# Kernel optimization log

Measured on AMD Instinct MI355X. Metric: run time of the kernel, lower is better.

## Reference

```python
import jax, jax.numpy as jnp
import numpy as np
from jax import lax

T_STEPS = 10       # fixed unroll length in forward (range(10))
TASK = 16          # params['task_size']
FEAT = 256         # input_size - task_size
VOCAB = 128        # params['vocab_size']
SH = 512           # sender_hidden_size
RH = 512           # receiver_hidden_size
ND = 10            # num_digits
B = 16384          # batch_size


def _gru_step(h, x, Wih, Whh, bih, bhh):
    # PyTorch GRU/GRUCell equations. Wih: [3H, In], Whh: [3H, H]
    gi = x @ Wih.T + bih
    gh = h @ Whh.T + bhh
    ir, iz, inn = jnp.split(gi, 3, axis=-1)
    hr, hz, hn = jnp.split(gh, 3, axis=-1)
    r = jax.nn.sigmoid(ir + hr)
    z = jax.nn.sigmoid(iz + hz)
    n = jnp.tanh(inn + r * hn)
    return (1.0 - z) * n + z * h


def setup_inputs() -> dict:
    key = jax.random.key(0)
    ks = jax.random.split(key, 16)
    s = 0.05
    x = jax.random.normal(ks[0], (B, TASK + FEAT), jnp.float32)
    u = jax.random.uniform(ks[1], (T_STEPS, B, VOCAB), jnp.float32, 1e-6, 1.0 - 1e-6)
    gumbel = -jnp.log(-jnp.log(u))  # standard Gumbel noise, fixed for determinism
    inp = {
        "x": x,
        "gumbel": gumbel,
        "W_in": jax.random.normal(ks[2], (SH, FEAT), jnp.float32) * s,
        "b_in": jnp.zeros((SH,), jnp.float32),
        "Wih_s": jax.random.normal(ks[3], (3 * SH, VOCAB), jnp.float32) * s,
        "Whh_s": jax.random.normal(ks[4], (3 * SH, SH), jnp.float32) * s,
        "bih_s": jnp.zeros((3 * SH,), jnp.float32),
        "bhh_s": jnp.zeros((3 * SH,), jnp.float32),
        "W_sp": jax.random.normal(ks[5], (VOCAB, SH), jnp.float32) * s,
        "b_sp": jnp.zeros((VOCAB,), jnp.float32),
        "Wih_r": jax.random.normal(ks[6], (3 * RH, VOCAB), jnp.float32) * s,
        "Whh_r": jax.random.normal(ks[7], (3 * RH, RH), jnp.float32) * s,
        "bih_r": jnp.zeros((3 * RH,), jnp.float32),
        "bhh_r": jnp.zeros((3 * RH,), jnp.float32),
        "W_c": jax.random.normal(ks[8], (ND, RH + TASK), jnp.float32) * s,
        "b_c": jnp.zeros((ND,), jnp.float32),
    }
    return inp


def _forward(x, gumbel, W_in, b_in, Wih_s, Whh_s, bih_s, bhh_s, W_sp, b_sp,
             Wih_r, Whh_r, bih_r, bhh_r, W_c, b_c):
    feats = x[:, TASK:]
    task = x[:, :TASK]
    h0 = jnp.tanh(feats @ W_in.T + b_in)                      # [B, SH]
    inp0 = jnp.zeros((x.shape[0], VOCAB), x.dtype)

    def sender_step(carry, g):
        h, w = carry
        h = _gru_step(h, w, Wih_s, Whh_s, bih_s, bhh_s)
        logits = h @ W_sp.T + b_sp
        y_soft = jax.nn.softmax(logits + g, axis=-1)          # gumbel_softmax, tau=1
        onehot = jax.nn.one_hot(jnp.argmax(y_soft, axis=-1), VOCAB, dtype=y_soft.dtype)
        y = onehot + y_soft - lax.stop_gradient(y_soft)       # hard straight-through
        return (h, lax.stop_gradient(y)), y                   # input_word = y.detach()

    (_, _), output_words = lax.scan(sender_step, (h0, inp0), gumbel)  # [10, B, V]

    # cumulative stop-token masking: once argmax==0 at step i-1, zero all steps >= i
    words = jnp.argmax(output_words, axis=2)                  # [10, B]
    nz = (words != 0).astype(output_words.dtype)
    alive = jnp.concatenate(
        [jnp.ones((1, words.shape[1]), output_words.dtype), jnp.cumprod(nz[:-1], axis=0)],
        axis=0)                                               # [10, B]
    masked = output_words * alive[:, :, None]

    # receiver GRU, zero initial hidden, return final hidden
    hr0 = jnp.zeros((x.shape[0], RH), x.dtype)

    def recv_step(h, w):
        h = _gru_step(h, w, Wih_r, Whh_r, bih_r, bhh_r)
        return h, None

    h_n, _ = lax.scan(recv_step, hr0, masked)                 # [B, RH]
    score = jnp.concatenate([h_n, task], axis=1) @ W_c.T + b_c  # [B, ND]
    return score


def reference(x, gumbel, W_in, b_in, Wih_s, Whh_s, bih_s, bhh_s, W_sp, b_sp,
              Wih_r, Whh_r, bih_r, bhh_r, W_c, b_c):
    return _forward(x, gumbel, W_in, b_in, Wih_s, Whh_s, bih_s, bhh_s, W_sp, b_sp,
                    Wih_r, Whh_r, bih_r, bhh_r, W_c, b_c)
```

## Files before the change

kernel.cpp:

```cpp
#include <hip/hip_runtime.h>
#include <math.h>

#define NB 16384
#define NT 10

typedef _Float16 f16;
typedef f16 f16x8 __attribute__((ext_vector_type(8)));
typedef f16 f16x4 __attribute__((ext_vector_type(4)));
typedef float f32x4 __attribute__((ext_vector_type(4)));

__device__ __forceinline__ float sigm_mid(float v) { return 1.0f / (1.0f + __expf(-v)); }
__device__ __forceinline__ float tanh_mid(float v) { return 1.0f - 2.0f / (1.0f + __expf(2.0f * v)); }
__device__ __forceinline__ float sigm_fast(float v) {
    return __builtin_amdgcn_rcpf(1.0f + __expf(-v));
}
__device__ __forceinline__ float tanh_fast(float v) {
    return 1.0f - 2.0f * __builtin_amdgcn_rcpf(1.0f + __expf(2.0f * v));
}

__device__ __forceinline__ void async_cp16(const f16* g, f16* l) {
    __builtin_amdgcn_global_load_lds(
        (const __attribute__((address_space(1))) unsigned int*)g,
        (__attribute__((address_space(3))) unsigned int*)l, 16, 0, 0);
}

__global__ __launch_bounds__(256) void wsplit_kernel(
    const float* __restrict__ W, f16* __restrict__ whi, f16* __restrict__ wlo,
    int rows, int kstride)
{
    const int u = blockIdx.x * 256 + threadIdx.x;
    const int kg = u / rows, row = u - kg * rows;
    const float* s = W + (size_t)row * kstride + kg * 8;
    f16x8 hi8, lo8;
    #pragma unroll
    for (int i = 0; i < 8; ++i) {
        float v = s[i];
        f16 hv = (f16)v;
        hi8[i] = hv;
        lo8[i] = (f16)(v - (float)hv);
    }
    *(f16x8*)&whi[(size_t)u * 8] = hi8;
    *(f16x8*)&wlo[(size_t)u * 8] = lo8;
}

__global__ __launch_bounds__(256) void xsplit_kernel(
    const float* __restrict__ x, f16* __restrict__ xhi, f16* __restrict__ xlo)
{
    const int u = blockIdx.x * 256 + threadIdx.x;
    const int kg = u >> 14, row = u & (NB - 1);
    const float* s = x + (size_t)row * 272 + 16 + kg * 8;
    f16x8 hi8, lo8;
    #pragma unroll
    for (int i = 0; i < 8; ++i) {
        float v = s[i];
        f16 hv = (f16)v;
        hi8[i] = hv;
        lo8[i] = (f16)(v - (float)hv);
    }
    *(f16x8*)&xhi[(size_t)u * 8] = hi8;
    *(f16x8*)&xlo[(size_t)u * 8] = lo8;
}

__global__ __launch_bounds__(256) void wihT_kernel(
    const float* __restrict__ Wih, float* __restrict__ WihT)
{
    const int u = blockIdx.x * 256 + threadIdx.x;
    const int w = u / 1536, c = u - w * 1536;
    WihT[u] = Wih[(size_t)c * 128 + w];
}

__global__ __launch_bounds__(256, 2) void h0_mfma(
    const f16* __restrict__ xs_hi, const f16* __restrict__ xs_lo,
    const f16* __restrict__ win_hi, const f16* __restrict__ win_lo,
    const float* __restrict__ bias, f16* __restrict__ h_hi, f16* __restrict__ h_lo)
{
    constexpr int UNITS = 1536;
    __shared__ __align__(16) f16 lds[2 * UNITS * 8];
    const int t = threadIdx.x;
    const int lane = t & 63, wave = t >> 6;
    const int wm = wave >> 1, wn = wave & 1;
    const int nid = (blockIdx.x & 7) * 128 + (blockIdx.x >> 3);
    const int m0 = (nid >> 3) * 128;
    const int n0 = (nid & 7) * 64;
    const int wbase = t & 192;

    const f32x4 z4 = {0.f, 0.f, 0.f, 0.f};
    f32x4 acc[4][2];
    #pragma unroll
    for (int mi = 0; mi < 4; ++mi)
        #pragma unroll
        for (int ni = 0; ni < 2; ++ni) acc[mi][ni] = z4;

    const int asel = ((lane >> 4) << 7) + wm * 64 + (lane & 15);
    const int bsel = ((lane >> 4) << 6) + wn * 32 + (lane & 15);

    const f16* sp[6];
    #pragma unroll
    for (int i = 0; i < 6; ++i) {
        const int u = i * 256 + t;
        const f16* src;
        if (u < 512) {
            src = xs_hi + ((size_t)(u >> 7) * NB + m0 + (u & 127)) * 8;
        } else if (u < 1024) {
            const int v = u - 512;
            src = xs_lo + ((size_t)(v >> 7) * NB + m0 + (v & 127)) * 8;
        } else if (u < 1280) {
            const int v = u - 1024;
            src = win_hi + ((size_t)(v >> 6) * 512 + n0 + (v & 63)) * 8;
        } else {
            const int v = u - 1280;
            src = win_lo + ((size_t)(v >> 6) * 512 + n0 + (v & 63)) * 8;
        }
        sp[i] = src;
    }

    #define H0_STAGE(buf_) { \
        f16* lb_ = lds + ((size_t)(buf_) * UNITS + wbase) * 8; \
        _Pragma("unroll") \
        for (int i = 0; i < 6; ++i) { \
            async_cp16(sp[i], lb_ + (size_t)i * 256 * 8); \
            sp[i] += (i < 4) ? (size_t)NB * 32 : (size_t)16384; \
        } \
    }

    H0_STAGE(0);
    asm volatile("s_waitcnt vmcnt(0)" ::: "memory");
    __syncthreads();

    for (int kb = 0; kb < 8; ++kb) {
        if (kb < 7) H0_STAGE((kb + 1) & 1);

        const f16* lb = lds + (size_t)(kb & 1) * UNITS * 8;
        f16x8 ah[4], al[4];
        #pragma unroll
        for (int mi = 0; mi < 4; ++mi) {
            ah[mi] = *(const f16x8*)&lb[(size_t)(asel + mi * 16) * 8];
            al[mi] = *(const f16x8*)&lb[(size_t)(512 + asel + mi * 16) * 8];
        }
        f16x8 bh[2], bl[2];
        #pragma unroll
        for (int ni = 0; ni < 2; ++ni) {
            bh[ni] = *(const f16x8*)&lb[(size_t)(1024 + bsel + ni * 16) * 8];
            bl[ni] = *(const f16x8*)&lb[(size_t)(1280 + bsel + ni * 16) * 8];
        }
        #pragma unroll
        for (int mi = 0; mi < 4; ++mi)
            #pragma unroll
            for (int ni = 0; ni < 2; ++ni) {
                acc[mi][ni] = __builtin_amdgcn_mfma_f32_16x16x32_f16(ah[mi], bh[ni], acc[mi][ni], 0, 0, 0);
                acc[mi][ni] = __builtin_amdgcn_mfma_f32_16x16x32_f16(ah[mi], bl[ni], acc[mi][ni], 0, 0, 0);
                acc[mi][ni] = __builtin_amdgcn_mfma_f32_16x16x32_f16(al[mi], bh[ni], acc[mi][ni], 0, 0, 0);
            }
        __syncthreads();
    }

    const int colb = n0 + wn * 32 + (lane & 15);
    const int rowb = m0 + wm * 64 + ((lane >> 4) << 2);
    #pragma unroll
    for (int ni = 0; ni < 2; ++ni) {
        const int col = colb + ni * 16;
        const float bb = bias[col];
        const size_t cbase = (size_t)(col >> 3) * NB * 8 + (col & 7);
        #pragma unroll
        for (int mi = 0; mi < 4; ++mi) {
            #pragma unroll
            for (int j = 0; j < 4; ++j) {
                const int r = rowb + mi * 16 + j;
                const float o = tanhf(acc[mi][ni][j] + bb);
                const f16 hh = (f16)o;
                const size_t idx = cbase + (size_t)r * 8;
                h_hi[idx] = hh;
                h_lo[idx] = (f16)(o - (float)hh);
            }
        }
    }
}

#define INIT_SP() { \
    _Pragma("unroll") \
    for (int i = 0; i < NST; ++i) { \
        const int u = i * 256 + t; \
        const f16* src; \
        if (PURE) { \
            if (u < 512) { \
                src = hc_hi + ((size_t)(u >> 7) * NB + m0 + (u & 127)) * 8; \
            } else { \
                const int w = u - 512; \
                src = w_hi + ((size_t)((w >> 6) & 3) * 1536 + (w >> 8) * 512 + n0 + (w & 63)) * 8; \
            } \
        } else { \
            if (u < 1024) { \
                const int v = u & 511; \
                const f16* hp = (u < 512) ? hc_hi : hc_lo; \
                src = hp + ((size_t)(v >> 7) * NB + m0 + (v & 127)) * 8; \
            } else { \
                const int v = u - 1024; \
                const f16* wp = (v < 768) ? w_hi : w_lo; \
                const int w = (v < 768) ? v : v - 768; \
                src = wp + ((size_t)((w >> 6) & 3) * 1536 + (w >> 8) * 512 + n0 + (w & 63)) * 8; \
            } \
        } \
        sp[i] = src; \
    } \
}
#define STAGE(buf_) { \
    f16* lb_ = lds + ((size_t)(buf_) * UNITS + wbase) * 8; \
    _Pragma("unroll") \
    for (int i = 0; i < NST; ++i) { \
        async_cp16(sp[i], lb_ + (size_t)i * 256 * 8); \
        sp[i] += (i < HCNT) ? (size_t)NB * 32 : (size_t)49152; \
    } \
}

template <int HZERO, int PURE>
__global__ __launch_bounds__(256, 2) void fused_gru(
    const f16* __restrict__ hc_hi, const f16* __restrict__ hc_lo,
    f16* __restrict__ hn_hi, f16* __restrict__ hn_lo,
    const f16* __restrict__ w_hi, const f16* __restrict__ w_lo,
    const float* __restrict__ WihT,
    const float* __restrict__ bih, const float* __restrict__ bhh,
    const int* __restrict__ wsel)
{
    constexpr int UNITS = PURE ? 1280 : 2560;
    constexpr int NST = PURE ? 5 : 10;
    constexpr int HCNT = PURE ? 2 : 4;
    __shared__ __align__(16) f16 lds[2 * UNITS * 8];
    const int t = threadIdx.x;
    const int lane = t & 63, wave = t >> 6;
    const int wm = wave >> 1, wn = wave & 1;
    const int nid = (blockIdx.x & 7) * 128 + (blockIdx.x >> 3);
    const int m0 = (nid >> 3) * 128;
    const int n0 = (nid & 7) * 64;
    const int wbase = t & 192;

    const f32x4 z4 = {0.f, 0.f, 0.f, 0.f};
    f32x4 acc[3][4][2];
    #pragma unroll
    for (int g = 0; g < 3; ++g)
        #pragma unroll
        for (int mi = 0; mi < 4; ++mi)
            #pragma unroll
            for (int ni = 0; ni < 2; ++ni) acc[g][mi][ni] = z4;

    float hold[2][4][4];
    #pragma unroll
    for (int ni = 0; ni < 2; ++ni)
        #pragma unroll
        for (int mi = 0; mi < 4; ++mi)
            #pragma unroll
            for (int j = 0; j < 4; ++j) hold[ni][mi][j] = 0.f;

    if (!HZERO) {
        const int asel = ((lane >> 4) << 7) + wm * 64 + (lane & 15);
        const int bsel = ((lane >> 4) << 6) + wn * 32 + (lane & 15);
        constexpr int B0 = PURE ? 512 : 1024;
        const int kbE = (n0 >> 5) + wn;
        const int kglA = (lane & 15) >> 3;
        const int rowlA = wm * 64 + ((lane >> 4) << 2);
        const int elemA = lane & 7;

        const f16* sp[NST];
        INIT_SP();
        STAGE(0);
        asm volatile("s_waitcnt vmcnt(0)" ::: "memory");
        __syncthreads();

        for (int kb = 0; kb < 16; ++kb) {
            if (kb < 15) STAGE((kb + 1) & 1);

            const f16* lb = lds + (size_t)(kb & 1) * UNITS * 8;
            f16x8 ah[4], al[4];
            #pragma unroll
            for (int mi = 0; mi < 4; ++mi) {
                ah[mi] = *(const f16x8*)&lb[(size_t)(asel + mi * 16) * 8];
                if (!PURE) al[mi] = *(const f16x8*)&lb[(size_t)(512 + asel + mi * 16) * 8];
            }
            #pragma unroll
            for (int g = 0; g < 3; ++g) {
                f16x8 bh[2], bl[2];
                #pragma unroll
                for (int ni = 0; ni < 2; ++ni) {
                    bh[ni] = *(const f16x8*)&lb[(size_t)(B0 + g * 256 + bsel + ni * 16) * 8];
                    if (!PURE) bl[ni] = *(const f16x8*)&lb[(size_t)(1792 + g * 256 + bsel + ni * 16) * 8];
                }
                #pragma unroll
                for (int mi = 0; mi < 4; ++mi)
                    #pragma unroll
                    for (int ni = 0; ni < 2; ++ni) {
                        acc[g][mi][ni] = __builtin_amdgcn_mfma_f32_16x16x32_f16(ah[mi], bh[ni], acc[g][mi][ni], 0, 0, 0);
                        if (!PURE) {
                            acc[g][mi][ni] = __builtin_amdgcn_mfma_f32_16x16x32_f16(ah[mi], bl[ni], acc[g][mi][ni], 0, 0, 0);
                            acc[g][mi][ni] = __builtin_amdgcn_mfma_f32_16x16x32_f16(al[mi], bh[ni], acc[g][mi][ni], 0, 0, 0);
                        }
                    }
            }

            if (kb == kbE) {
                #pragma unroll
                for (int ni = 0; ni < 2; ++ni)
                    #pragma unroll
                    for (int mi = 0; mi < 4; ++mi)
                        #pragma unroll
                        for (int j = 0; j < 4; ++j) {
                            const int unit = (kglA + 2 * ni) * 128 + rowlA + mi * 16 + j;
                            float hv = (float)lb[(size_t)unit * 8 + elemA];
                            if (!PURE) hv += (float)lb[(size_t)(512 + unit) * 8 + elemA];
                            hold[ni][mi][j] = hv;
                        }
            }
            __syncthreads();
        }
    }

    const int colb = n0 + wn * 32 + (lane & 15);
    const int rowb = m0 + wm * 64 + ((lane >> 4) << 2);
    int wd[16];
    if (wsel) {
        #pragma unroll
        for (int mi = 0; mi < 4; ++mi) {
            const int4 w4 = *(const int4*)&wsel[rowb + mi * 16];
            wd[mi * 4 + 0] = w4.x; wd[mi * 4 + 1] = w4.y;
            wd[mi * 4 + 2] = w4.z; wd[mi * 4 + 3] = w4.w;
        }
    } else {
        #pragma unroll
        for (int i = 0; i < 16; ++i) wd[i] = -1;
    }

    #pragma unroll
    for (int ni = 0; ni < 2; ++ni) {
        const int col = colb + ni * 16;
        const float b_r = bih[col], b_z = bih[512 + col], b_n = bih[1024 + col];
        const float c_r = bhh[col], c_z = bhh[512 + col], c_n = bhh[1024 + col];
        const size_t cbase = (size_t)(col >> 3) * NB * 8 + (col & 7);
        #pragma unroll
        for (int mi = 0; mi < 4; ++mi) {
            #pragma unroll
            for (int j = 0; j < 4; ++j) {
                const int r = rowb + mi * 16 + j;
                const int word = wd[mi * 4 + j];
                float wir = 0.f, wiz = 0.f, win = 0.f;
                if (word >= 0) {
                    const float* wt = WihT + (size_t)word * 1536 + col;
                    wir = wt[0]; wiz = wt[512]; win = wt[1024];
                }
                const size_t idx = cbase + (size_t)r * 8;
                const float ra = wir + b_r + acc[0][mi][ni][j] + c_r;
                const float za = wiz + b_z + acc[1][mi][ni][j] + c_z;
                const float rr = PURE ? sigm_fast(ra) : sigm_mid(ra);
                const float zz = PURE ? sigm_fast(za) : sigm_mid(za);
                const float na = win + b_n + rr * (acc[2][mi][ni][j] + c_n);
                const float nn = PURE ? tanh_fast(na) : tanh_mid(na);
                const float hv = (1.f - zz) * nn + zz * hold[ni][mi][j];
                const f16 hh = (f16)hv;
                hn_hi[idx] = hh;
                if (!PURE) hn_lo[idx] = (f16)(hv - (float)hh);
            }
        }
    }
}

__global__ __launch_bounds__(256, 2) void argmax_mfma(
    const f16* __restrict__ h_hi, const f16* __restrict__ h_lo,
    const f16* __restrict__ wsp_hi, const f16* __restrict__ wsp_lo,
    const float* __restrict__ bsp, const float* __restrict__ gum,
    int* __restrict__ wout)
{
    __shared__ __align__(16) f16 lds[2 * 1536 * 8];
    const int t = threadIdx.x;
    const int lane = t & 63, wave = t >> 6;
    const int mBase = blockIdx.x * 64;

    const f32x4 z4 = {0.f, 0.f, 0.f, 0.f};
    f32x4 acc[8];
    #pragma unroll
    for (int nf = 0; nf < 8; ++nf) acc[nf] = z4;

    const f16* sp[6];
    sp[0] = h_hi   + ((size_t)(t >> 6) * NB + mBase + (t & 63)) * 8;
    sp[1] = h_lo   + ((size_t)(t >> 6) * NB + mBase + (t & 63)) * 8;
    sp[2] = wsp_hi + ((size_t)(t >> 7) * 128 + (t & 127)) * 8;
    sp[3] = wsp_hi + ((size_t)(2 + (t >> 7)) * 128 + (t & 127)) * 8;
    sp[4] = wsp_lo + ((size_t)(t >> 7) * 128 + (t & 127)) * 8;
    sp[5] = wsp_lo + ((size_t)(2 + (t >> 7)) * 128 + (t & 127)) * 8;

    f16x8 st[6];
    #pragma unroll
    for (int i = 0; i < 6; ++i) {
        st[i] = *(const f16x8*)sp[i];
        sp[i] += (i < 2) ? (size_t)NB * 32 : (size_t)4096;
    }

    const int aselU = (lane >> 4) * 64 + wave * 16 + (lane & 15);
    const int bselU = 512 + (lane >> 4) * 128 + (lane & 15);

    for (int kb = 0; kb < 16; ++kb) {
        f16* lb = lds + (size_t)(kb & 1) * 1536 * 8;
        #pragma unroll
        for (int i = 0; i < 6; ++i)
            *(f16x8*)&lb[(size_t)(i * 256 + t) * 8] = st[i];
        __syncthreads();
        if (kb < 15) {
            #pragma unroll
            for (int i = 0; i < 6; ++i) {
                st[i] = *(const f16x8*)sp[i];
                sp[i] += (i < 2) ? (size_t)NB * 32 : (size_t)4096;
            }
        }

        f16x8 ah = *(const f16x8*)&lb[(size_t)aselU * 8];
        f16x8 al = *(const f16x8*)&lb[(size_t)(256 + aselU) * 8];
        #pragma unroll
        for (int nf = 0; nf < 8; ++nf) {
            f16x8 bh = *(const f16x8*)&lb[(size_t)(bselU + nf * 16) * 8];
            f16x8 bl = *(const f16x8*)&lb[(size_t)(512 + bselU + nf * 16) * 8];
            acc[nf] = __builtin_amdgcn_mfma_f32_16x16x32_f16(ah, bh, acc[nf], 0, 0, 0);
            acc[nf] = __builtin_amdgcn_mfma_f32_16x16x32_f16(ah, bl, acc[nf], 0, 0, 0);
            acc[nf] = __builtin_amdgcn_mfma_f32_16x16x32_f16(al, bh, acc[nf], 0, 0, 0);
        }
    }

    float bv[4];
    int bi[4];
    #pragma unroll
    for (int j = 0; j < 4; ++j) { bv[j] = -1e30f; bi[j] = 0; }
    const int rw0 = mBase + wave * 16 + ((lane >> 4) << 2);
    #pragma unroll
    for (int nf = 0; nf < 8; ++nf) {
        const int col = (lane & 15) + nf * 16;
        const float bb = bsp[col];
        #pragma unroll
        for (int j = 0; j < 4; ++j) {
            const float v = acc[nf][j] + bb + gum[(size_t)(rw0 + j) * 128 + col];
            if (v > bv[j] || (v == bv[j] && col < bi[j])) { bv[j] = v; bi[j] = col; }
        }
    }
    #pragma unroll
    for (int j = 0; j < 4; ++j) {
        #pragma unroll
        for (int off = 1; off <= 8; off <<= 1) {
            const float ov = __shfl_xor(bv[j], off, 64);
            const int oi = __shfl_xor(bi[j], off, 64);
            if (ov > bv[j] || (ov == bv[j] && oi < bi[j])) { bv[j] = ov; bi[j] = oi; }
        }
        if ((lane & 15) == 0) wout[rw0 + j] = bi[j];
    }
}

__global__ __launch_bounds__(256) void eff_kernel(
    const int* __restrict__ words, int* __restrict__ eff)
{
    const int b = blockIdx.x * 256 + threadIdx.x;
    int alive = 1;
    #pragma unroll
    for (int t = 0; t < NT; ++t) {
        const int w = words[(size_t)t * NB + b];
        eff[(size_t)t * NB + b] = alive ? w : -1;
        alive = alive & (w != 0);
    }
}

__global__ __launch_bounds__(256) void score_kernel(
    const f16* __restrict__ h_hi,
    const float* __restrict__ x, const float* __restrict__ Wc,
    const float* __restrict__ bc, float* __restrict__ out)
{
    __shared__ float Wcs[10][528];
    const int t = threadIdx.x;
    for (int q = t; q < 1320; q += 256)
        *(float4*)&(((float*)Wcs)[q * 4]) = *(const float4*)&Wc[q * 4];
    __syncthreads();

    const int row = blockIdx.x * 256 + t;
    float acc[10];
    #pragma unroll
    for (int d = 0; d < 10; ++d) acc[d] = 0.f;

    for (int kg = 0; kg < 64; ++kg) {
        f16x8 vh = *(const f16x8*)&h_hi[((size_t)kg * NB + row) * 8];
        #pragma unroll
        for (int i = 0; i < 8; ++i) {
            const float v = (float)vh[i];
            #pragma unroll
            for (int d = 0; d < 10; ++d) acc[d] += v * Wcs[d][kg * 8 + i];
        }
    }
    #pragma unroll
    for (int j = 0; j < 16; ++j) {
        const float tv = x[(size_t)row * 272 + j];
        #pragma unroll
        for (int d = 0; d < 10; ++d) acc[d] += tv * Wcs[d][512 + j];
    }
    #pragma unroll
    for (int d = 0; d < 10; ++d) out[(size_t)row * 10 + d] = acc[d] + bc[d];
}

extern "C" void kernel_launch(void* const* d_in, const int* in_sizes, int n_in,
                              void* d_out, int out_size, void* d_ws, size_t ws_size,
                              hipStream_t stream) {
    const float* x      = (const float*)d_in[0];
    const float* gumbel = (const float*)d_in[1];
    const float* W_in   = (const float*)d_in[2];
    const float* b_in   = (const float*)d_in[3];
    const float* Wih_s  = (const float*)d_in[4];
    const float* Whh_s  = (const float*)d_in[5];
    const float* bih_s  = (const float*)d_in[6];
    const float* bhh_s  = (const float*)d_in[7];
    const float* W_sp   = (const float*)d_in[8];
    const float* b_sp   = (const float*)d_in[9];
    const float* Wih_r  = (const float*)d_in[10];
    const float* Whh_r  = (const float*)d_in[11];
    const float* bih_r  = (const float*)d_in[12];
    const float* bhh_r  = (const float*)d_in[13];
    const float* W_c    = (const float*)d_in[14];
    const float* b_c    = (const float*)d_in[15];
    float* out = (float*)d_out;

    char* base = (char*)d_ws;
    f16* S_hi[2], *S_lo[2];
    S_hi[0] = (f16*)(base);
    S_lo[0] = (f16*)(base + 16777216);
    S_hi[1] = (f16*)(base + 33554432);
    S_lo[1] = (f16*)(base + 50331648);
    f16* R0 = (f16*)(base);
    f16* R1 = (f16*)(base + 16777216);
    f16* ws_s_hi = (f16*)(base + 67108864);
    f16* ws_s_lo = (f16*)(base + 68681728);
    f16* ws_r_hi = (f16*)(base + 70254592);
    f16* ws_r_lo = (f16*)(base + 71827456);
    float* wihT_s = (float*)(base + 73400320);
    float* wihT_r = (float*)(base + 74186752);
    int* words   = (int*)(base + 74973184);
    int* eff     = (int*)(base + 75628544);
    f16* wsp_hi  = (f16*)(base + 76283904);
    f16* wsp_lo  = (f16*)(base + 76414976);
    f16* xs_hi   = (f16*)(base + 76546048);
    f16* xs_lo   = (f16*)(base + 84934656);
    f16* win_hi  = (f16*)(base + 93323264);
    f16* win_lo  = (f16*)(base + 93585408);

    const dim3 blk(256);
    const dim3 gFus(NB / 128 * 8);

    wsplit_kernel<<<dim3(384), blk, 0, stream>>>(Whh_s, ws_s_hi, ws_s_lo, 1536, 512);
    wsplit_kernel<<<dim3(384), blk, 0, stream>>>(Whh_r, ws_r_hi, ws_r_lo, 1536, 512);
    wsplit_kernel<<<dim3(32), blk, 0, stream>>>(W_sp, wsp_hi, wsp_lo, 128, 512);
    wsplit_kernel<<<dim3(64), blk, 0, stream>>>(W_in, win_hi, win_lo, 512, 256);
    xsplit_kernel<<<dim3(2048), blk, 0, stream>>>(x, xs_hi, xs_lo);
    wihT_kernel<<<dim3(768), blk, 0, stream>>>(Wih_s, wihT_s);
    wihT_kernel<<<dim3(768), blk, 0, stream>>>(Wih_r, wihT_r);

    h0_mfma<<<gFus, blk, 0, stream>>>(xs_hi, xs_lo, win_hi, win_lo, b_in, S_hi[0], S_lo[0]);
    int cur = 0;

    for (int t = 0; t < NT; ++t) {
        const int* wprev = (t == 0) ? (const int*)nullptr : (words + (size_t)(t - 1) * NB);
        const int nxt = cur ^ 1;
        fused_gru<0, 0><<<gFus, blk, 0, stream>>>(
            S_hi[cur], S_lo[cur], S_hi[nxt], S_lo[nxt],
            ws_s_hi, ws_s_lo, wihT_s, bih_s, bhh_s, wprev);
        cur = nxt;
        argmax_mfma<<<dim3(NB / 64), blk, 0, stream>>>(
            S_hi[cur], S_lo[cur], wsp_hi, wsp_lo,
            b_sp, gumbel + (size_t)t * NB * 128, words + (size_t)t * NB);
    }
    eff_kernel<<<dim3(NB / 256), blk, 0, stream>>>(words, eff);

    fused_gru<1, 1><<<gFus, blk, 0, stream>>>(
        R1, R1, R0, R0, ws_r_hi, ws_r_lo, wihT_r, bih_r, bhh_r, eff);
    for (int t = 1; t < NT; ++t) {
        f16* rin  = (t & 1) ? R0 : R1;
        f16* rout = (t & 1) ? R1 : R0;
        fused_gru<0, 1><<<gFus, blk, 0, stream>>>(
            rin, rin, rout, rout, ws_r_hi, ws_r_lo, wihT_r, bih_r, bhh_r,
            eff + (size_t)t * NB);
    }

    score_kernel<<<dim3(NB / 256), blk, 0, stream>>>(R1, x, W_c, b_c, out);
}
```

Measured before the change: 1.453 ms.

## Load weight fragments directly from global memory instead of staging through LDS

In the h0, fused GRU and argmax kernels, weight (B-operand) fragments are now read straight from global memory into registers per k-block instead of being async-copied into LDS. Only the activation tiles are staged in LDS, which shrinks the shared-memory footprint and the number of async copies per stage. The argmax kernel also switches from register-staged stores to async global-to-LDS double buffering. The trade-off is that the weight loads are now synchronous global/L2 reads on the MFMA critical path, and are repeated by every wave that needs them rather than shared once through LDS.

```diff
diff --git a/kernel.cpp b/kernel.cpp
--- a/kernel.cpp
+++ b/kernel.cpp
@@ -74,7 +74,7 @@
     const f16* __restrict__ win_hi, const f16* __restrict__ win_lo,
     const float* __restrict__ bias, f16* __restrict__ h_hi, f16* __restrict__ h_lo)
 {
-    constexpr int UNITS = 1536;
+    constexpr int UNITS = 1024;
     __shared__ __align__(16) f16 lds[2 * UNITS * 8];
     const int t = threadIdx.x;
     const int lane = t & 63, wave = t >> 6;
@@ -92,34 +92,25 @@
         for (int ni = 0; ni < 2; ++ni) acc[mi][ni] = z4;
 
     const int asel = ((lane >> 4) << 7) + wm * 64 + (lane & 15);
-    const int bsel = ((lane >> 4) << 6) + wn * 32 + (lane & 15);
-
-    const f16* sp[6];
-    #pragma unroll
-    for (int i = 0; i < 6; ++i) {
+    const size_t boff = ((size_t)(lane >> 4) * 512 + n0 + wn * 32 + (lane & 15)) * 8;
+    const f16* bph = win_hi + boff;
+    const f16* bpl = win_lo + boff;
+
+    const f16* sp[4];
+    #pragma unroll
+    for (int i = 0; i < 4; ++i) {
         const int u = i * 256 + t;
-        const f16* src;
-        if (u < 512) {
-            src = xs_hi + ((size_t)(u >> 7) * NB + m0 + (u & 127)) * 8;
-        } else if (u < 1024) {
-            const int v = u - 512;
-            src = xs_lo + ((size_t)(v >> 7) * NB + m0 + (v & 127)) * 8;
-        } else if (u < 1280) {
-            const int v = u - 1024;
-            src = win_hi + ((size_t)(v >> 6) * 512 + n0 + (v & 63)) * 8;
-        } else {
-            const int v = u - 1280;
-            src = win_lo + ((size_t)(v >> 6) * 512 + n0 + (v & 63)) * 8;
-        }
-        sp[i] = src;
+        const int v = u & 511;
+        const f16* hp = (u < 512) ? xs_hi : xs_lo;
+        sp[i] = hp + ((size_t)(v >> 7) * NB + m0 + (v & 127)) * 8;
     }
 
     #define H0_STAGE(buf_) { \
         f16* lb_ = lds + ((size_t)(buf_) * UNITS + wbase) * 8; \
         _Pragma("unroll") \
-        for (int i = 0; i < 6; ++i) { \
+        for (int i = 0; i < 4; ++i) { \
             async_cp16(sp[i], lb_ + (size_t)i * 256 * 8); \
-            sp[i] += (i < 4) ? (size_t)NB * 32 : (size_t)16384; \
+            sp[i] += (size_t)NB * 32; \
         } \
     }
 
@@ -140,9 +131,11 @@
         f16x8 bh[2], bl[2];
         #pragma unroll
         for (int ni = 0; ni < 2; ++ni) {
-            bh[ni] = *(const f16x8*)&lb[(size_t)(1024 + bsel + ni * 16) * 8];
-            bl[ni] = *(const f16x8*)&lb[(size_t)(1280 + bsel + ni * 16) * 8];
-        }
+            bh[ni] = *(const f16x8*)(bph + (size_t)ni * 128);
+            bl[ni] = *(const f16x8*)(bpl + (size_t)ni * 128);
+        }
+        bph += (size_t)4 * 512 * 8;
+        bpl += (size_t)4 * 512 * 8;
         #pragma unroll
         for (int mi = 0; mi < 4; ++mi)
             #pragma unroll
@@ -180,27 +173,10 @@
     _Pragma("unroll") \
     for (int i = 0; i < NST; ++i) { \
         const int u = i * 256 + t; \
-        const f16* src; \
-        if (PURE) { \
-            if (u < 512) { \
-                src = hc_hi + ((size_t)(u >> 7) * NB + m0 + (u & 127)) * 8; \
-            } else { \
-                const int w = u - 512; \
-                src = w_hi + ((size_t)((w >> 6) & 3) * 1536 + (w >> 8) * 512 + n0 + (w & 63)) * 8; \
-            } \
-        } else { \
-            if (u < 1024) { \
-                const int v = u & 511; \
-                const f16* hp = (u < 512) ? hc_hi : hc_lo; \
-                src = hp + ((size_t)(v >> 7) * NB + m0 + (v & 127)) * 8; \
-            } else { \
-                const int v = u - 1024; \
-                const f16* wp = (v < 768) ? w_hi : w_lo; \
-                const int w = (v < 768) ? v : v - 768; \
-                src = wp + ((size_t)((w >> 6) & 3) * 1536 + (w >> 8) * 512 + n0 + (w & 63)) * 8; \
-            } \
-        } \
-        sp[i] = src; \
+        const f16* hp; int v; \
+        if (PURE) { hp = hc_hi; v = u; } \
+        else { v = u & 511; hp = (u < 512) ? hc_hi : hc_lo; } \
+        sp[i] = hp + ((size_t)(v >> 7) * NB + m0 + (v & 127)) * 8; \
     } \
 }
 #define STAGE(buf_) { \
@@ -208,7 +184,7 @@
     _Pragma("unroll") \
     for (int i = 0; i < NST; ++i) { \
         async_cp16(sp[i], lb_ + (size_t)i * 256 * 8); \
-        sp[i] += (i < HCNT) ? (size_t)NB * 32 : (size_t)49152; \
+        sp[i] += (size_t)NB * 32; \
     } \
 }
 
@@ -221,9 +197,8 @@
     const float* __restrict__ bih, const float* __restrict__ bhh,
     const int* __restrict__ wsel)
 {
-    constexpr int UNITS = PURE ? 1280 : 2560;
-    constexpr int NST = PURE ? 5 : 10;
-    constexpr int HCNT = PURE ? 2 : 4;
+    constexpr int UNITS = PURE ? 512 : 1024;
+    constexpr int NST = PURE ? 2 : 4;
     __shared__ __align__(16) f16 lds[2 * UNITS * 8];
     const int t = threadIdx.x;
     const int lane = t & 63, wave = t >> 6;
@@ -252,8 +227,9 @@
 
     if (!HZERO) {
         const int asel = ((lane >> 4) << 7) + wm * 64 + (lane & 15);
-        const int bsel = ((lane >> 4) << 6) + wn * 32 + (lane & 15);
-        constexpr int B0 = PURE ? 512 : 1024;
+        const size_t boff = ((size_t)(lane >> 4) * 1536 + n0 + wn * 32 + (lane & 15)) * 8;
+        const f16* bph = w_hi + boff;
+        const f16* bpl = PURE ? (const f16*)nullptr : (w_lo + boff);
         const int kbE = (n0 >> 5) + wn;
         const int kglA = (lane & 15) >> 3;
         const int rowlA = wm * 64 + ((lane >> 4) << 2);
@@ -280,8 +256,8 @@
                 f16x8 bh[2], bl[2];
                 #pragma unroll
                 for (int ni = 0; ni < 2; ++ni) {
-                    bh[ni] = *(const f16x8*)&lb[(size_t)(B0 + g * 256 + bsel + ni * 16) * 8];
-                    if (!PURE) bl[ni] = *(const f16x8*)&lb[(size_t)(1792 + g * 256 + bsel + ni * 16) * 8];
+                    bh[ni] = *(const f16x8*)(bph + (size_t)(g * 512 + ni * 16) * 8);
+                    if (!PURE) bl[ni] = *(const f16x8*)(bpl + (size_t)(g * 512 + ni * 16) * 8);
                 }
                 #pragma unroll
                 for (int mi = 0; mi < 4; ++mi)
@@ -294,6 +270,8 @@
                         }
                     }
             }
+            bph += (size_t)4 * 1536 * 8;
+            if (!PURE) bpl += (size_t)4 * 1536 * 8;
 
             if (kb == kbE) {
                 #pragma unroll
@@ -366,58 +344,57 @@
     const float* __restrict__ bsp, const float* __restrict__ gum,
     int* __restrict__ wout)
 {
-    __shared__ __align__(16) f16 lds[2 * 1536 * 8];
+    constexpr int UNITS = 512;
+    __shared__ __align__(16) f16 lds[2 * UNITS * 8];
     const int t = threadIdx.x;
     const int lane = t & 63, wave = t >> 6;
     const int mBase = blockIdx.x * 64;
+    const int wbase = t & 192;
 
     const f32x4 z4 = {0.f, 0.f, 0.f, 0.f};
     f32x4 acc[8];
     #pragma unroll
     for (int nf = 0; nf < 8; ++nf) acc[nf] = z4;
 
-    const f16* sp[6];
-    sp[0] = h_hi   + ((size_t)(t >> 6) * NB + mBase + (t & 63)) * 8;
-    sp[1] = h_lo   + ((size_t)(t >> 6) * NB + mBase + (t & 63)) * 8;
-    sp[2] = wsp_hi + ((size_t)(t >> 7) * 128 + (t & 127)) * 8;
-    sp[3] = wsp_hi + ((size_t)(2 + (t >> 7)) * 128 + (t & 127)) * 8;
-    sp[4] = wsp_lo + ((size_t)(t >> 7) * 128 + (t & 127)) * 8;
-    sp[5] = wsp_lo + ((size_t)(2 + (t >> 7)) * 128 + (t & 127)) * 8;
-
-    f16x8 st[6];
-    #pragma unroll
-    for (int i = 0; i < 6; ++i) {
-        st[i] = *(const f16x8*)sp[i];
-        sp[i] += (i < 2) ? (size_t)NB * 32 : (size_t)4096;
-    }
+    const f16* sp[2];
+    sp[0] = h_hi + ((size_t)(t >> 6) * NB + mBase + (t & 63)) * 8;
+    sp[1] = h_lo + ((size_t)(t >> 6) * NB + mBase + (t & 63)) * 8;
+
+    const size_t boff = ((size_t)(lane >> 4) * 128 + (lane & 15)) * 8;
+    const f16* bph = wsp_hi + boff;
+    const f16* bpl = wsp_lo + boff;
+
+    #define AM_STAGE(buf_) { \
+        f16* lb_ = lds + ((size_t)(buf_) * UNITS + wbase) * 8; \
+        async_cp16(sp[0], lb_); \
+        async_cp16(sp[1], lb_ + (size_t)256 * 8); \
+        sp[0] += (size_t)NB * 32; \
+        sp[1] += (size_t)NB * 32; \
+    }
+
+    AM_STAGE(0);
+    asm volatile("s_waitcnt vmcnt(0)" ::: "memory");
+    __syncthreads();
 
     const int aselU = (lane >> 4) * 64 + wave * 16 + (lane & 15);
-    const int bselU = 512 + (lane >> 4) * 128 + (lane & 15);
 
     for (int kb = 0; kb < 16; ++kb) {
-        f16* lb = lds + (size_t)(kb & 1) * 1536 * 8;
-        #pragma unroll
-        for (int i = 0; i < 6; ++i)
-            *(f16x8*)&lb[(size_t)(i * 256 + t) * 8] = st[i];
-        __syncthreads();
-        if (kb < 15) {
-            #pragma unroll
-            for (int i = 0; i < 6; ++i) {
-                st[i] = *(const f16x8*)sp[i];
-                sp[i] += (i < 2) ? (size_t)NB * 32 : (size_t)4096;
-            }
-        }
-
+        if (kb < 15) AM_STAGE((kb + 1) & 1);
+
+        const f16* lb = lds + (size_t)(kb & 1) * UNITS * 8;
         f16x8 ah = *(const f16x8*)&lb[(size_t)aselU * 8];
         f16x8 al = *(const f16x8*)&lb[(size_t)(256 + aselU) * 8];
         #pragma unroll
         for (int nf = 0; nf < 8; ++nf) {
-            f16x8 bh = *(const f16x8*)&lb[(size_t)(bselU + nf * 16) * 8];
-            f16x8 bl = *(const f16x8*)&lb[(size_t)(512 + bselU + nf * 16) * 8];
+            f16x8 bh = *(const f16x8*)(bph + (size_t)nf * 128);
+            f16x8 bl = *(const f16x8*)(bpl + (size_t)nf * 128);
             acc[nf] = __builtin_amdgcn_mfma_f32_16x16x32_f16(ah, bh, acc[nf], 0, 0, 0);
             acc[nf] = __builtin_amdgcn_mfma_f32_16x16x32_f16(ah, bl, acc[nf], 0, 0, 0);
             acc[nf] = __builtin_amdgcn_mfma_f32_16x16x32_f16(al, bh, acc[nf], 0, 0, 0);
         }
+        bph += (size_t)4 * 128 * 8;
+        bpl += (size_t)4 * 128 * 8;
+        __syncthreads();
     }
 
     float bv[4];
```

New measurement: 1.884 ms. 1.3x slower.
